# Optimization experiments

Measured on AMD Instinct MI355X. Metric: run time of the kernel, lower is better.

The kernel has to match this reference:

```python
import jax, jax.numpy as jnp
import numpy as np

H, W = 85, 85
N_HEAD = 8

def layernorm(x, g, b, eps=1e-5):
    m = x.mean(-1, keepdims=True)
    v = ((x - m) ** 2).mean(-1, keepdims=True)
    return (x - m) * jax.lax.rsqrt(v + eps) * g + b


def setup_inputs() -> dict:
    key = jax.random.key(0)
    ks = jax.random.split(key, 12)
    B, C = 8, 256
    N = H * W
    hd = C // N_HEAD
    Ch = C * 4  # mlp_ratio = 4
    init = lambda k, fan_in, sh: (jax.random.normal(k, sh, jnp.float32) / np.float32(np.sqrt(fan_in)))
    d = {}
    d['fx'] = jax.random.normal(ks[0], (B, N, C), jnp.float32)
    # ln_1
    d['ln1_g'] = jnp.ones((C,), jnp.float32); d['ln1_b'] = jnp.zeros((C,), jnp.float32)
    # Galerkin linear attention projections (per-head split of C)
    d['Wq'] = init(ks[1], C, (C, C)); d['bq'] = jnp.zeros((C,), jnp.float32)
    d['Wk'] = init(ks[2], C, (C, C)); d['bk'] = jnp.zeros((C,), jnp.float32)
    d['Wv'] = init(ks[3], C, (C, C)); d['bv'] = jnp.zeros((C,), jnp.float32)
    d['Wo'] = init(ks[4], C, (C, C)); d['bo'] = jnp.zeros((C,), jnp.float32)
    # per-head LayerNorms on K and V (Galerkin normalization replacing softmax)
    d['kln_g'] = jnp.ones((N_HEAD, hd), jnp.float32); d['kln_b'] = jnp.zeros((N_HEAD, hd), jnp.float32)
    d['vln_g'] = jnp.ones((N_HEAD, hd), jnp.float32); d['vln_b'] = jnp.zeros((N_HEAD, hd), jnp.float32)
    # ln_2
    d['ln2_g'] = jnp.ones((C,), jnp.float32); d['ln2_b'] = jnp.zeros((C,), jnp.float32)
    # MLP (n_layers=0, res=False): pre linear + gelu, post linear
    d['W1'] = init(ks[5], C, (C, Ch)); d['b1'] = jnp.zeros((Ch,), jnp.float32)
    d['W2'] = init(ks[6], Ch, (Ch, C)); d['b2'] = jnp.zeros((C,), jnp.float32)
    return d


def reference(fx, ln1_g, ln1_b, Wq, bq, Wk, bk, Wv, bv, Wo, bo,
              kln_g, kln_b, vln_g, vln_b, ln2_g, ln2_b, W1, b1, W2, b2):
    B, N, C = fx.shape
    hd = C // N_HEAD
    x = layernorm(fx, ln1_g, ln1_b)  # [B,N,C]
    # (permute/reshape to image grid and back is a no-op for per-token attention math)
    split = lambda t: t.reshape(B, N, N_HEAD, hd).transpose(0, 2, 1, 3)  # [B,h,N,d]
    q = split(x @ Wq + bq)
    k = split(x @ Wk + bk)
    v = split(x @ Wv + bv)
    # Galerkin: LayerNorm on K and V over head dim, no softmax
    k = layernorm(k, kln_g[None, :, None, :], kln_b[None, :, None, :])
    v = layernorm(v, vln_g[None, :, None, :], vln_b[None, :, None, :])
    kv = jnp.einsum('bhnd,bhne->bhde', k, v) / N  # [B,h,d,d]
    attn = jnp.einsum('bhnd,bhde->bhne', q, kv)   # [B,h,N,d]
    attn = attn.transpose(0, 2, 1, 3).reshape(B, N, C)
    attn = attn @ Wo + bo
    fx = fx + attn  # residual 1
    x2 = layernorm(fx, ln2_g, ln2_b)
    x2 = jax.nn.gelu(x2 @ W1 + b1) @ W2 + b2
    return fx + x2  # residual 2
```

## Files before the change

kernel.cpp:

```cpp
#include <hip/hip_runtime.h>
#include <hip/hip_bf16.h>
#include <stdint.h>

#define B_ 8
#define NTOK 7225
#define MTOT (B_*NTOK)
#define MROWS 58368
#define MLP_TILES 904
#define ATT_TILES 113

typedef unsigned short u16;
typedef u16 u16x8 __attribute__((ext_vector_type(8)));
typedef u16 u16x4 __attribute__((ext_vector_type(4)));
typedef __bf16 bf16x8 __attribute__((ext_vector_type(8)));
typedef float f32x4 __attribute__((ext_vector_type(4)));

__device__ inline float bf2f(u16 u){ union{float f;uint32_t i;}c; c.i=((uint32_t)u)<<16; return c.f; }
__device__ inline u16 f2bf(float f){ union{float f;uint32_t i;}c; c.f=f; uint32_t x=c.i;
                                     return (u16)((x + 0x7fffu + ((x>>16)&1u))>>16); }
__device__ inline uint32_t cvt_pk_bf16(float a, float b){
  uint32_t r; asm("v_cvt_pk_bf16_f32 %0, %1, %2" : "=v"(r) : "v"(a), "v"(b)); return r;
}
__device__ inline float gelu_f(float x){
  float t = 0.7978845608028654f * x * (1.0f + 0.044715f*x*x);
  float e = __expf(2.0f*t);
  return x * (1.0f - __builtin_amdgcn_rcpf(e + 1.0f));
}

__device__ inline void gload_lds16(const u16* g, u16* l) {
  __builtin_amdgcn_global_load_lds(
      (__attribute__((address_space(1))) void*)(const_cast<u16*>(g)),
      (__attribute__((address_space(3))) void*)(l), 16, 0, 0);
}

__global__ __launch_bounds__(512, 4)
void proj64(const u16* __restrict__ x2, const u16* __restrict__ Wt,
            const float* __restrict__ bias, u16* __restrict__ outp)
{
  __shared__ alignas(16) u16 Xs[16384];
  __shared__ alignas(16) u16 Wb[16384];
  __shared__ alignas(16) u16 Bb[4096];
  const int tid = threadIdx.x;
  const int wid = tid >> 6, lane = tid & 63;
  const int wm = wid >> 2, wn = wid & 3;
  const int lr = lane & 15, sl = lane >> 4;
  const long rowBase = (long)blockIdx.x * 64;

#pragma unroll
  for (int i = 0; i < 4; ++i) {
    const int u = i*512 + tid;
    const int r = u >> 5, pu = u & 31;
    gload_lds16(x2 + (rowBase + r)*256 + ((pu ^ (r & 31)) << 3), &Xs[u*8]);
  }
  auto stageW = [&](int c) {
#pragma unroll
    for (int i = 0; i < 4; ++i) {
      const int u = i*512 + tid;
      const int r = u >> 5, pu = u & 31;
      gload_lds16(Wt + (long)(c*64 + r)*256 + ((pu ^ (r & 31)) << 3), &Wb[u*8]);
    }
  };

  for (int c = 0; c < 8; ++c) {
    stageW(c);
    asm volatile("s_waitcnt vmcnt(0)" ::: "memory");
    __builtin_amdgcn_s_barrier();
    f32x4 acc[2] = {};
#pragma unroll
    for (int kk = 0; kk < 8; ++kk) {
      const int u = kk*4 + sl;
      const int rB = wn*16 + lr;
      bf16x8 wb = *reinterpret_cast<const bf16x8*>(&Wb[(rB*32 + (u ^ (rB & 31)))*8]);
#pragma unroll
      for (int mi = 0; mi < 2; ++mi) {
        const int rA = wm*32 + mi*16 + lr;
        bf16x8 xa = *reinterpret_cast<const bf16x8*>(&Xs[(rA*32 + (u ^ (rA & 31)))*8]);
        acc[mi] = __builtin_amdgcn_mfma_f32_16x16x32_bf16(wb, xa, acc[mi], 0, 0, 0);
      }
    }
#pragma unroll
    for (int mi = 0; mi < 2; ++mi) {
      const int r = wm*32 + mi*16 + lr;
      const int col = wn*16 + sl*4;
      f32x4 v = acc[mi] + *reinterpret_cast<const f32x4*>(&bias[c*64 + col]);
      uint2 pk; pk.x = cvt_pk_bf16(v[0], v[1]); pk.y = cvt_pk_bf16(v[2], v[3]);
      const int uw = (col >> 3) ^ (r & 7);
      *reinterpret_cast<uint2*>(&Bb[r*64 + uw*8 + (col & 7)]) = pk;
    }
    asm volatile("s_waitcnt lgkmcnt(0)" ::: "memory");
    __builtin_amdgcn_s_barrier();
    {
      const int r = tid >> 3, u = tid & 7;
      const int phys = u ^ (r & 7);
      u16x8 val = *reinterpret_cast<const u16x8*>(&Bb[r*64 + phys*8]);
      *reinterpret_cast<u16x8*>(outp + (rowBase + r)*512 + c*64 + u*8) = val;
    }
  }
}

__global__ __launch_bounds__(512, 4)
void att64(const u16* __restrict__ x2, const u16* __restrict__ Watt,
           const float* __restrict__ be, const float* __restrict__ fx,
           float* __restrict__ outF, u16* __restrict__ x2out,
           const float* __restrict__ g2, const float* __restrict__ b2)
{
  __shared__ alignas(16) u16 Xs[16384];
  __shared__ alignas(16) u16 Wb[16384];
  __shared__ float Rb[512];
  const int tid = threadIdx.x;
  const int wid = tid >> 6, lane = tid & 63;
  const int wm = wid >> 2, wn = wid & 3;
  const int lr = lane & 15, sl = lane >> 4;
  const int bx = blockIdx.x, bz = blockIdx.y;
  const long rowBase = (long)bz * NTOK + (long)bx * 64;
  const int rowsLeft = NTOK - bx * 64;
  const u16* Wt = Watt + (long)bz * 65536;
  const float* beP = be + bz * 256;

#pragma unroll
  for (int i = 0; i < 4; ++i) {
    const int u = i*512 + tid;
    const int r = u >> 5, pu = u & 31;
    gload_lds16(x2 + (rowBase + r)*256 + ((pu ^ (r & 31)) << 3), &Xs[u*8]);
  }
  auto stageW = [&](int c) {
#pragma unroll
    for (int i = 0; i < 4; ++i) {
      const int u = i*512 + tid;
      const int r = u >> 5, pu = u & 31;
      gload_lds16(Wt + (long)(c*64 + r)*256 + ((pu ^ (r & 31)) << 3), &Wb[u*8]);
    }
  };

  uint2 pk[4][2];
  float sacc[2] = {0.f, 0.f}, qacc[2] = {0.f, 0.f};

#pragma unroll
  for (int c = 0; c < 4; ++c) {
    stageW(c);
    asm volatile("s_waitcnt vmcnt(0)" ::: "memory");
    __builtin_amdgcn_s_barrier();
    f32x4 acc[2] = {};
#pragma unroll
    for (int kk = 0; kk < 8; ++kk) {
      const int u = kk*4 + sl;
      const int rB = wn*16 + lr;
      bf16x8 wb = *reinterpret_cast<const bf16x8*>(&Wb[(rB*32 + (u ^ (rB & 31)))*8]);
#pragma unroll
      for (int mi = 0; mi < 2; ++mi) {
        const int rA = wm*32 + mi*16 + lr;
        bf16x8 xa = *reinterpret_cast<const bf16x8*>(&Xs[(rA*32 + (u ^ (rA & 31)))*8]);
        acc[mi] = __builtin_amdgcn_mfma_f32_16x16x32_bf16(wb, xa, acc[mi], 0, 0, 0);
      }
    }
#pragma unroll
    for (int mi = 0; mi < 2; ++mi) {
      const int r = wm*32 + mi*16 + lr;
      const bool valid = (r < rowsLeft);
      const int col = c*64 + wn*16 + sl*4;
      const long oidx = (rowBase + r)*256 + col;
      f32x4 rv = valid ? *reinterpret_cast<const f32x4*>(&fx[oidx])
                       : f32x4{0.f,0.f,0.f,0.f};
      f32x4 v = acc[mi] + *reinterpret_cast<const f32x4*>(&beP[col]) + rv;
      if (valid) *reinterpret_cast<f32x4*>(&outF[oidx]) = v;
      sacc[mi] += v[0]+v[1]+v[2]+v[3];
      qacc[mi] += v[0]*v[0]+v[1]*v[1]+v[2]*v[2]+v[3]*v[3];
      pk[c][mi].x = cvt_pk_bf16(v[0], v[1]);
      pk[c][mi].y = cvt_pk_bf16(v[2], v[3]);
    }
    asm volatile("s_waitcnt lgkmcnt(0)" ::: "memory");
    __builtin_amdgcn_s_barrier();
  }

#pragma unroll
  for (int mi = 0; mi < 2; ++mi) {
    float s = sacc[mi], q = qacc[mi];
    s += __shfl_xor(s, 16); s += __shfl_xor(s, 32);
    q += __shfl_xor(q, 16); q += __shfl_xor(q, 32);
    if (sl == 0) {
      const int r = wm*32 + mi*16 + lr;
      Rb[      wn*64 + r] = s;
      Rb[256 + wn*64 + r] = q;
    }
  }
  __syncthreads();
#pragma unroll
  for (int mi = 0; mi < 2; ++mi) {
    const int r = wm*32 + mi*16 + lr;
    if (r >= rowsLeft) continue;
    const float s_t = Rb[r] + Rb[64 + r] + Rb[128 + r] + Rb[192 + r];
    const float q_t = Rb[256 + r] + Rb[320 + r] + Rb[384 + r] + Rb[448 + r];
    const float m = s_t * (1.0f/256.0f);
    const float var = q_t * (1.0f/256.0f) - m*m;
    const float rs = rsqrtf(var + 1e-5f);
    const long growb = (rowBase + r)*256;
#pragma unroll
    for (int c = 0; c < 4; ++c) {
      const int col = c*64 + wn*16 + sl*4;
      const f32x4 gv = *reinterpret_cast<const f32x4*>(&g2[col]);
      const f32x4 bv = *reinterpret_cast<const f32x4*>(&b2[col]);
      float v0 = bf2f((u16)(pk[c][mi].x & 0xffffu));
      float v1 = bf2f((u16)(pk[c][mi].x >> 16));
      float v2 = bf2f((u16)(pk[c][mi].y & 0xffffu));
      float v3 = bf2f((u16)(pk[c][mi].y >> 16));
      uint2 o;
      o.x = cvt_pk_bf16((v0 - m)*rs*gv[0] + bv[0], (v1 - m)*rs*gv[1] + bv[1]);
      o.y = cvt_pk_bf16((v2 - m)*rs*gv[2] + bv[2], (v3 - m)*rs*gv[3] + bv[3]);
      *reinterpret_cast<uint2*>(x2out + growb + col) = o;
    }
  }
}

__global__ __launch_bounds__(512, 4)
void mlp_fused4(const u16* __restrict__ x2, const u16* __restrict__ W1t,
                const u16* __restrict__ W2t, const float* __restrict__ b1,
                const float* __restrict__ b2, float* __restrict__ outF,
                int rowsValid)
{
  __shared__ alignas(16) u16 Xs[64*256];
  __shared__ alignas(16) u16 Wb[16384];
  __shared__ alignas(16) u16 Hs[64*64];
  const int tid = threadIdx.x;
  const int wid = tid >> 6, lane = tid & 63;
  const int wm = wid >> 2, wn = wid & 3;
  const int lr = lane & 15, sl = lane >> 4;
  const long rowBase = (long)blockIdx.x * 64;

#pragma unroll
  for (int i = 0; i < 4; ++i) {
    const int u = i*512 + tid;
    const int r = u >> 5, pu = u & 31;
    gload_lds16(x2 + (rowBase + r)*256 + ((pu ^ (r & 31)) << 3), &Xs[u*8]);
  }
  auto stageW1 = [&](int c) {
#pragma unroll
    for (int i = 0; i < 4; ++i) {
      const int u = i*512 + tid;
      const int r = u >> 5, pu = u & 31;
      gload_lds16(W1t + (long)(c*64 + r)*256 + ((pu ^ (r & 31)) << 3), &Wb[u*8]);
    }
  };
  auto stageW2 = [&](int c) {
#pragma unroll
    for (int i = 0; i < 4; ++i) {
      const int u = i*512 + tid;
      const int r = u >> 3, pu = u & 7;
      gload_lds16(W2t + (long)r*1024 + c*64 + ((pu ^ (r & 7)) << 3), &Wb[u*8]);
    }
  };
  stageW1(0);
  asm volatile("s_waitcnt vmcnt(0)" ::: "memory");
  __syncthreads();

  f32x4 acc2[2][4] = {};
  for (int c = 0; c < 16; ++c) {
    f32x4 acc1[2] = {};
#pragma unroll
    for (int kk = 0; kk < 8; ++kk) {
      const int u = kk*4 + sl;
      const int rB = wn*16 + lr;
      bf16x8 wb = *reinterpret_cast<const bf16x8*>(&Wb[(rB*32 + (u ^ (rB & 31)))*8]);
#pragma unroll
      for (int mi = 0; mi < 2; ++mi) {
        const int rA = wm*32 + mi*16 + lr;
        bf16x8 xa = *reinterpret_cast<const bf16x8*>(&Xs[(rA*32 + (u ^ (rA & 31)))*8]);
        acc1[mi] = __builtin_amdgcn_mfma_f32_16x16x32_bf16(wb, xa, acc1[mi], 0, 0, 0);
      }
    }
    const float* b1c = b1 + c*64;
#pragma unroll
    for (int mi = 0; mi < 2; ++mi) {
      const int r = wm*32 + mi*16 + lr;
      const int col = wn*16 + sl*4;
      f32x4 v = acc1[mi] + *reinterpret_cast<const f32x4*>(&b1c[col]);
      uint2 pk; pk.x = cvt_pk_bf16(gelu_f(v[0]), gelu_f(v[1]));
      pk.y = cvt_pk_bf16(gelu_f(v[2]), gelu_f(v[3]));
      const int uw = (col >> 3) ^ (r & 7);
      *reinterpret_cast<uint2*>(&Hs[r*64 + uw*8 + (col & 7)]) = pk;
    }
    asm volatile("s_waitcnt lgkmcnt(0)" ::: "memory");
    __builtin_amdgcn_s_barrier();
    stageW2(c);
    asm volatile("s_waitcnt vmcnt(0)" ::: "memory");
    __builtin_amdgcn_s_barrier();

#pragma unroll
    for (int kk2 = 0; kk2 < 2; ++kk2) {
      const int u = kk2*4 + sl;
      bf16x8 ha[2];
#pragma unroll
      for (int mi = 0; mi < 2; ++mi) {
        const int r = wm*32 + mi*16 + lr;
        ha[mi] = *reinterpret_cast<const bf16x8*>(&Hs[(r*8 + (u ^ (r & 7)))*8]);
      }
#pragma unroll
      for (int nj = 0; nj < 4; ++nj) {
        const int rB = wn*64 + nj*16 + lr;
        bf16x8 wb = *reinterpret_cast<const bf16x8*>(&Wb[(rB*8 + (u ^ (rB & 7)))*8]);
#pragma unroll
        for (int mi = 0; mi < 2; ++mi)
          acc2[mi][nj] = __builtin_amdgcn_mfma_f32_16x16x32_bf16(wb, ha[mi], acc2[mi][nj], 0, 0, 0);
      }
    }
    __builtin_amdgcn_s_barrier();
    if (c + 1 < 16) {
      stageW1(c + 1);
      asm volatile("s_waitcnt vmcnt(0)" ::: "memory");
      __builtin_amdgcn_s_barrier();
    }
  }
#pragma unroll
  for (int mi = 0; mi < 2; ++mi) {
    const int r = wm*32 + mi*16 + lr;
    if (rowBase + r < rowsValid) {
      float* orow = outF + (rowBase + r)*256;
#pragma unroll
      for (int nj = 0; nj < 4; ++nj) {
        const int col = wn*64 + nj*16 + sl*4;
        f32x4 v = acc2[mi][nj] + *reinterpret_cast<const f32x4*>(&b2[col])
                + *reinterpret_cast<const f32x4*>(&orow[col]);
        *reinterpret_cast<f32x4*>(&orow[col]) = v;
      }
    }
  }
}

__global__ __launch_bounds__(256)
void ln_kernel(const float* __restrict__ in, const float* __restrict__ g,
               const float* __restrict__ bt, u16* __restrict__ out, int M)
{
  const int wv = threadIdx.x >> 6, lane = threadIdx.x & 63;
  const int t = blockIdx.x * 4 + wv;
  if (t >= M) return;
  const float4 x = reinterpret_cast<const float4*>(in + (long)t*256)[lane];
  float s = x.x + x.y + x.z + x.w;
  float q = x.x*x.x + x.y*x.y + x.z*x.z + x.w*x.w;
#pragma unroll
  for (int o = 32; o > 0; o >>= 1) { s += __shfl_xor(s, o); q += __shfl_xor(q, o); }
  const float m  = s * (1.0f/256.0f);
  const float var = q * (1.0f/256.0f) - m*m;
  const float rs = rsqrtf(var + 1e-5f);
  const float4 gv = reinterpret_cast<const float4*>(g)[lane];
  const float4 bv = reinterpret_cast<const float4*>(bt)[lane];
  uint2 o4;
  o4.x = cvt_pk_bf16((x.x - m)*rs*gv.x + bv.x, (x.y - m)*rs*gv.y + bv.y);
  o4.y = cvt_pk_bf16((x.z - m)*rs*gv.z + bv.z, (x.w - m)*rs*gv.w + bv.w);
  *reinterpret_cast<uint2*>(out + (long)t*256 + lane*4) = o4;
}

__global__ __launch_bounds__(256)
void kv_kernel(const u16* __restrict__ KV,
               const float* __restrict__ kg, const float* __restrict__ kb,
               const float* __restrict__ vg, const float* __restrict__ vb,
               float* __restrict__ kvout)
{
  const int bh = blockIdx.x, b = bh >> 3, h = bh & 7;
  const int tid = threadIdx.x;
  __shared__ u16 kls[256][32];
  __shared__ u16 vls[256][32];
  __shared__ float sg[4][32];
  if (tid < 32) {
    sg[0][tid] = kg[h*32 + tid];
    sg[1][tid] = kb[h*32 + tid];
    sg[2][tid] = vg[h*32 + tid];
    sg[3][tid] = vb[h*32 + tid];
  }
  const int d = tid >> 3, e0 = (tid & 7) * 4;
  float a0=0, a1=0, a2=0, a3=0;

  for (int sub = 0; sub < 2; ++sub) {
    const int r = blockIdx.y * 512 + sub * 256 + tid;
    __syncthreads();
    if (r < NTOK) {
      const u16* rowp = KV + (long)(b*NTOK + r)*512;
#pragma unroll
      for (int kv2 = 0; kv2 < 2; ++kv2) {
        const u16* p = rowp + (kv2 ? 256 : 0) + h*32;
        float xv[32]; float s = 0.f;
#pragma unroll
        for (int q4 = 0; q4 < 4; ++q4) {
          u16x8 u = *reinterpret_cast<const u16x8*>(p + q4*8);
#pragma unroll
          for (int j = 0; j < 8; ++j) { float f = bf2f(u[j]); xv[q4*8+j] = f; s += f; }
        }
        const float m = s * (1.0f/32.0f);
        float vv = 0.f;
#pragma unroll
        for (int j = 0; j < 32; ++j) { float d2 = xv[j]-m; vv += d2*d2; }
        const float rs = rsqrtf(vv*(1.0f/32.0f) + 1e-5f);
        const float* gg = sg[kv2 ? 2 : 0];
        const float* bb = sg[kv2 ? 3 : 1];
        u16 (*dst)[32] = kv2 ? vls : kls;
#pragma unroll
        for (int j = 0; j < 32; ++j) dst[tid][j] = f2bf((xv[j]-m)*rs*gg[j] + bb[j]);
      }
    } else {
#pragma unroll
      for (int j = 0; j < 32; ++j) { kls[tid][j] = 0; vls[tid][j] = 0; }
    }
    __syncthreads();
#pragma unroll 4
    for (int rr = 0; rr < 256; ++rr) {
      const float kd = bf2f(kls[rr][d]);
      u16x4 v4 = *reinterpret_cast<const u16x4*>(&vls[rr][e0]);
      a0 += kd * bf2f(v4[0]); a1 += kd * bf2f(v4[1]);
      a2 += kd * bf2f(v4[2]); a3 += kd * bf2f(v4[3]);
    }
  }
  const float sc = 1.0f / (float)NTOK;
  float* o = kvout + (long)bh*1024 + d*32 + e0;
  atomicAdd(o+0, a0*sc); atomicAdd(o+1, a1*sc);
  atomicAdd(o+2, a2*sc); atomicAdd(o+3, a3*sc);
}

__global__ __launch_bounds__(256)
void woeff_kernel(const float* __restrict__ kv, const float* __restrict__ Wo,
                  u16* __restrict__ Woet)
{
  const int b = blockIdx.x >> 8, c = blockIdx.x & 255;
  const int rtid = threadIdx.x;
  const int h = rtid >> 5, dd = rtid & 31;
  const float* kvp = kv + ((long)(b*8 + h)*32 + dd)*32;
  float s = 0.f;
#pragma unroll 8
  for (int e = 0; e < 32; ++e) s += kvp[e] * Wo[(h*32 + e)*256 + c];
  Woet[(long)(b*256 + c)*256 + rtid] = f2bf(s);
}

__global__ __launch_bounds__(256)
void watt_kernel(const u16* __restrict__ wq_bf, const u16* __restrict__ Woet,
                 u16* __restrict__ Watt)
{
  const int b = blockIdx.x >> 8, c = blockIdx.x & 255;
  const int k = threadIdx.x;
  const u16* wr = wq_bf + (long)k*256;
  const u16* er = Woet + ((long)(b*256 + c))*256;
  float s = 0.f;
#pragma unroll 4
  for (int j0 = 0; j0 < 256; j0 += 8) {
    u16x8 wv = *reinterpret_cast<const u16x8*>(wr + j0);
    u16x8 ev = *reinterpret_cast<const u16x8*>(er + j0);
#pragma unroll
    for (int j = 0; j < 8; ++j) s += bf2f(wv[j]) * bf2f(ev[j]);
  }
  Watt[((long)(b*256 + c))*256 + k] = f2bf(s);
}

__global__ __launch_bounds__(256)
void be_kernel(const float* __restrict__ bq, const float* __restrict__ bo,
               const u16* __restrict__ Woet, float* __restrict__ be)
{
  const int b = blockIdx.x, c = threadIdx.x;
  const u16* er = Woet + ((long)(b*256 + c))*256;
  float s = bo[c];
#pragma unroll 4
  for (int j0 = 0; j0 < 256; j0 += 8) {
    u16x8 ev = *reinterpret_cast<const u16x8*>(er + j0);
#pragma unroll
    for (int j = 0; j < 8; ++j) s += bq[j0+j] * bf2f(ev[j]);
  }
  be[b*256 + c] = s;
}

__device__ void transpose_tile(const float* __restrict__ src, u16* __restrict__ dst,
                               int R, int C, int tcx, int trY)
{
  __shared__ float t[32][33];
  const int tc = tcx * 32, tr = trY * 32;
  const int lx = threadIdx.x & 31, ly = threadIdx.x >> 5;
#pragma unroll
  for (int i = 0; i < 32; i += 8)
    t[ly + i][lx] = src[(long)(tr + ly + i)*C + tc + lx];
  __syncthreads();
#pragma unroll
  for (int i = 0; i < 32; i += 8)
    dst[(long)(tc + ly + i)*R + tr + lx] = f2bf(t[lx][ly + i]);
}

__global__ __launch_bounds__(256)
void prep_kernel(const float* __restrict__ Wk, const float* __restrict__ Wv,
                 const float* __restrict__ W1, const float* __restrict__ W2,
                 const float* __restrict__ Wq,
                 const float* __restrict__ bk, const float* __restrict__ bv,
                 u16* __restrict__ Wkv_t, u16* __restrict__ W1_t, u16* __restrict__ W2_t,
                 u16* __restrict__ wq_bf, float* __restrict__ kvb, float* __restrict__ bkv)
{
  int b = blockIdx.x;
  if (b < 256)      { transpose_tile(W1, W1_t, 256, 1024, b & 31, b >> 5); }
  else if (b < 512) { b -= 256; transpose_tile(W2, W2_t, 1024, 256, b & 7, b >> 3); }
  else if (b < 576) { b -= 512; transpose_tile(Wk, Wkv_t,         256, 256, b & 7, b >> 3); }
  else if (b < 640) { b -= 576; transpose_tile(Wv, Wkv_t + 65536, 256, 256, b & 7, b >> 3); }
  else if (b < 648) {
    const int base = (b - 640) * 8192 + threadIdx.x;
#pragma unroll
    for (int i = 0; i < 32; ++i) wq_bf[base + i*256] = f2bf(Wq[base + i*256]);
  } else if (b < 656) {
    const int base = (b - 648) * 8192 + threadIdx.x;
#pragma unroll
    for (int i = 0; i < 32; ++i) kvb[base + i*256] = 0.f;
  } else {
    const int i = threadIdx.x;
    bkv[i] = bk[i]; bkv[256 + i] = bv[i];
  }
}

extern "C" void kernel_launch(void* const* d_in, const int* in_sizes, int n_in,
                              void* d_out, int out_size, void* d_ws, size_t ws_size,
                              hipStream_t stream)
{
  const float* fx    = (const float*)d_in[0];
  const float* ln1_g = (const float*)d_in[1];
  const float* ln1_b = (const float*)d_in[2];
  const float* Wq = (const float*)d_in[3];
  const float* bq = (const float*)d_in[4];
  const float* Wk = (const float*)d_in[5];
  const float* bk = (const float*)d_in[6];
  const float* Wv = (const float*)d_in[7];
  const float* bv = (const float*)d_in[8];
  const float* Wo = (const float*)d_in[9];
  const float* bo = (const float*)d_in[10];
  const float* kg  = (const float*)d_in[11];
  const float* kbb = (const float*)d_in[12];
  const float* vg  = (const float*)d_in[13];
  const float* vbb = (const float*)d_in[14];
  const float* ln2_g = (const float*)d_in[15];
  const float* ln2_b = (const float*)d_in[16];
  const float* W1 = (const float*)d_in[17];
  const float* b1 = (const float*)d_in[18];
  const float* W2 = (const float*)d_in[19];
  const float* b2 = (const float*)d_in[20];
  float* outF = (float*)d_out;

  char* ws = (char*)d_ws;
  size_t off = 0;
  auto alloc = [&](size_t bytes) { char* p = ws + off; off += (bytes + 255) & ~(size_t)255; return p; };
  u16* bufX   = (u16*)alloc((size_t)MROWS*256*2);
  u16* bufKV  = (u16*)alloc((size_t)MROWS*512*2);
  u16* Wkv_t  = (u16*)alloc(512*256*2);
  u16* W1_t   = (u16*)alloc(1024*256*2);
  u16* W2_t   = (u16*)alloc(256*1024*2);
  u16* Woe_t  = (u16*)alloc((size_t)8*256*256*2);
  u16* Watt   = (u16*)alloc((size_t)8*256*256*2);
  u16* wq_bf  = (u16*)alloc(256*256*2);
  float* kvb  = (float*)alloc((size_t)64*1024*4);
  float* bkv  = (float*)alloc(512*4);
  float* be   = (float*)alloc(8*256*4);
  (void)ws_size; (void)out_size; (void)n_in; (void)in_sizes;

  prep_kernel<<<657, 256, 0, stream>>>(Wk, Wv, W1, W2, Wq, bk, bv,
                                       Wkv_t, W1_t, W2_t, wq_bf, kvb, bkv);

  ln_kernel<<<MTOT/4, 256, 0, stream>>>(fx, ln1_g, ln1_b, bufX, MTOT);

  proj64<<<MLP_TILES, 512, 0, stream>>>(bufX, Wkv_t, bkv, bufKV);

  kv_kernel<<<dim3(64, 15), 256, 0, stream>>>(bufKV, kg, kbb, vg, vbb, kvb);

  woeff_kernel<<<2048, 256, 0, stream>>>(kvb, Wo, Woe_t);
  watt_kernel<<<2048, 256, 0, stream>>>(wq_bf, Woe_t, Watt);
  be_kernel<<<8, 256, 0, stream>>>(bq, bo, Woe_t, be);

  att64<<<dim3(ATT_TILES, 8), 512, 0, stream>>>(
      bufX, Watt, be, fx, outF, bufX, ln2_g, ln2_b);

  mlp_fused4<<<MLP_TILES, 512, 0, stream>>>(bufX, W1_t, W2_t, b1, b2, outF, MTOT);
}
```

Baseline: 294.2 us.

## Prefetch MLP weight chunks into registers to overlap global loads with MFMA

Replaces the synchronous global-to-LDS staging of W1 and W2 chunks with register prefetch. Each W2 chunk is loaded into registers at the start of the iteration, hidden behind the first GEMM, and the next W1 chunk is loaded while the second GEMM runs. The registers are then written to LDS, which removes the full vmcnt(0) stalls at every barrier. The cost is extra VGPR pressure from the eight u16x8 buffers, which could hurt occupancy under launch_bounds(512,4).

```diff
diff --git a/kernel.cpp b/kernel.cpp
--- a/kernel.cpp
+++ b/kernel.cpp
@@ -217,43 +217,44 @@
                 const float* __restrict__ b2, float* __restrict__ outF,
                 int rowsValid)
 {
-  __shared__ alignas(16) u16 Xs[64*256];
+  __shared__ alignas(16) u16 Xs[16384];
   __shared__ alignas(16) u16 Wb[16384];
-  __shared__ alignas(16) u16 Hs[64*64];
+  __shared__ alignas(16) u16 Hs[4096];
   const int tid = threadIdx.x;
   const int wid = tid >> 6, lane = tid & 63;
   const int wm = wid >> 2, wn = wid & 3;
   const int lr = lane & 15, sl = lane >> 4;
   const long rowBase = (long)blockIdx.x * 64;
 
+  u16x8 w1r[4];
+#pragma unroll
+  for (int i = 0; i < 4; ++i) {
+    const int u = i*512 + tid;
+    const int r = u >> 5, pu = u & 31;
+    w1r[i] = *reinterpret_cast<const u16x8*>(W1t + (long)r*256 + ((pu ^ (r & 31)) << 3));
+  }
 #pragma unroll
   for (int i = 0; i < 4; ++i) {
     const int u = i*512 + tid;
     const int r = u >> 5, pu = u & 31;
     gload_lds16(x2 + (rowBase + r)*256 + ((pu ^ (r & 31)) << 3), &Xs[u*8]);
   }
-  auto stageW1 = [&](int c) {
-#pragma unroll
-    for (int i = 0; i < 4; ++i) {
-      const int u = i*512 + tid;
-      const int r = u >> 5, pu = u & 31;
-      gload_lds16(W1t + (long)(c*64 + r)*256 + ((pu ^ (r & 31)) << 3), &Wb[u*8]);
-    }
-  };
-  auto stageW2 = [&](int c) {
+#pragma unroll
+  for (int i = 0; i < 4; ++i)
+    *reinterpret_cast<u16x8*>(&Wb[(i*512 + tid)*8]) = w1r[i];
+  asm volatile("s_waitcnt vmcnt(0) lgkmcnt(0)" ::: "memory");
+  __syncthreads();
+
+  f32x4 acc2[2][4] = {};
+  for (int c = 0; c < 16; ++c) {
+    const bool st = (c + 1 < 16);
+    u16x8 w2r[4];
 #pragma unroll
     for (int i = 0; i < 4; ++i) {
       const int u = i*512 + tid;
       const int r = u >> 3, pu = u & 7;
-      gload_lds16(W2t + (long)r*1024 + c*64 + ((pu ^ (r & 7)) << 3), &Wb[u*8]);
-    }
-  };
-  stageW1(0);
-  asm volatile("s_waitcnt vmcnt(0)" ::: "memory");
-  __syncthreads();
-
-  f32x4 acc2[2][4] = {};
-  for (int c = 0; c < 16; ++c) {
+      w2r[i] = *reinterpret_cast<const u16x8*>(W2t + (long)r*1024 + c*64 + ((pu ^ (r & 7)) << 3));
+    }
     f32x4 acc1[2] = {};
 #pragma unroll
     for (int kk = 0; kk < 8; ++kk) {
@@ -280,8 +281,18 @@
     }
     asm volatile("s_waitcnt lgkmcnt(0)" ::: "memory");
     __builtin_amdgcn_s_barrier();
-    stageW2(c);
-    asm volatile("s_waitcnt vmcnt(0)" ::: "memory");
+#pragma unroll
+    for (int i = 0; i < 4; ++i)
+      *reinterpret_cast<u16x8*>(&Wb[(i*512 + tid)*8]) = w2r[i];
+    if (st) {
+#pragma unroll
+      for (int i = 0; i < 4; ++i) {
+        const int u = i*512 + tid;
+        const int r = u >> 5, pu = u & 31;
+        w1r[i] = *reinterpret_cast<const u16x8*>(W1t + (long)((c+1)*64 + r)*256 + ((pu ^ (r & 31)) << 3));
+      }
+    }
+    asm volatile("s_waitcnt lgkmcnt(0)" ::: "memory");
     __builtin_amdgcn_s_barrier();
 
 #pragma unroll
@@ -303,9 +314,11 @@
       }
     }
     __builtin_amdgcn_s_barrier();
-    if (c + 1 < 16) {
-      stageW1(c + 1);
-      asm volatile("s_waitcnt vmcnt(0)" ::: "memory");
+    if (st) {
+#pragma unroll
+      for (int i = 0; i < 4; ++i)
+        *reinterpret_cast<u16x8*>(&Wb[(i*512 + tid)*8]) = w1r[i];
+      asm volatile("s_waitcnt lgkmcnt(0)" ::: "memory");
       __builtin_amdgcn_s_barrier();
     }
   }
```

Measured after the change: 301.0 us. +2.3%, slower.
